# Kernel tuning notes

Measured on AMD Instinct MI355X. Metric: run time of the kernel, lower is better.

## Reference

```python
import jax, jax.numpy as jnp
import numpy as np

HIDDEN = 4096
NUM_BLOCKS = 8
BLOCK = HIDDEN // NUM_BLOCKS  # 512


def setup_inputs() -> dict:
    key = jax.random.key(0)
    k1, k2, k3, k4 = jax.random.split(key, 4)
    return {
        "weight": jax.random.normal(k1, (HIDDEN, HIDDEN), dtype=jnp.float32) * 0.02,
        "bias": jax.random.normal(k2, (HIDDEN,), dtype=jnp.float32) * 0.02,
        "x": jax.random.normal(k3, (4, 2048, HIDDEN), dtype=jnp.float32),
        "proj_R": jax.random.normal(k4, (NUM_BLOCKS, BLOCK, BLOCK), dtype=jnp.float32) * 0.02,
        "layer_idx": 0,
    }


def _cayley_batch(A):
    # Q = (I - S) @ inv(I + S + 1e-6*I), S = 0.5*(A - A^T), batched over blocks
    r = A.shape[-1]
    I = jnp.eye(r, dtype=A.dtype)
    S = 0.5 * (A - jnp.swapaxes(A, -2, -1))
    Minv = jnp.linalg.inv(I + S + 1e-6 * I)
    return jnp.einsum('bij,bjk->bik', I - S, Minv)


def reference(weight, bias, x, proj_R, layer_idx):
    Q = _cayley_batch(proj_R)                     # [nb, bs, bs], orthogonal blocks
    nb, bs, _ = Q.shape
    # block_diag(Q) @ weight == batched block-row matmul (off-diagonal blocks are zero)
    Wb = weight.reshape(nb, bs, weight.shape[1])  # [nb, bs, in]
    filt = jnp.einsum('bij,bjk->bik', Q, Wb).reshape(nb * bs, weight.shape[1])
    # F.linear(x, filt, bias)
    return jnp.einsum('bsi,oi->bso', x, filt) + bias
```

## Files before the change

### kernel.cpp

```cpp
#include <hip/hip_runtime.h>

typedef unsigned short u16;
typedef __attribute__((ext_vector_type(8))) short bf16x8;
typedef __attribute__((ext_vector_type(4))) float f32x4;
typedef __attribute__((ext_vector_type(8))) unsigned short u16x8;
typedef __attribute__((ext_vector_type(4))) unsigned short u16x4;

__device__ __forceinline__ u16 f2bf(float f){
  unsigned int u = __builtin_bit_cast(unsigned int, f);
  u += 0x7FFFu + ((u >> 16) & 1u);
  return (u16)(u >> 16);
}
__device__ __forceinline__ float bf2f(u16 h){
  unsigned int u = ((unsigned int)h) << 16;
  return __builtin_bit_cast(float, u);
}

__device__ __forceinline__ void load16(const u16* g, u16* s){
  __builtin_amdgcn_global_load_lds((const __attribute__((address_space(1))) unsigned int*)g,
                                   (__attribute__((address_space(3))) unsigned int*)s,
                                   16, 0, 0);
}

__global__ __launch_bounds__(256) void build_s(const float* __restrict__ R, u16* __restrict__ Sbf,
                                               u16* __restrict__ Dbf){
  int idx = blockIdx.x * 256 + threadIdx.x;
  int b = idx >> 18;
  int i = (idx >> 9) & 511;
  int j = idx & 511;
  float a  = R[idx];
  float at = R[(b << 18) + (j << 9) + i];
  float s = 0.5f * (a - at);
  Sbf[idx] = f2bf(s);
  Dbf[idx] = f2bf((i == j ? 2.000003f : 0.0f) - 2.000001f * s);
}

__global__ __launch_bounds__(256) void conv_bf16(const float* __restrict__ src, u16* __restrict__ dst){
  size_t i = (size_t)blockIdx.x * 256 + threadIdx.x;
  const float4* s = (const float4*)src + i * 2;
  float4 v0 = s[0], v1 = s[1];
  u16x8 o = { f2bf(v0.x), f2bf(v0.y), f2bf(v0.z), f2bf(v0.w),
              f2bf(v1.x), f2bf(v1.y), f2bf(v1.z), f2bf(v1.w) };
  *(u16x8*)(dst + i * 8) = o;
}

__global__ __launch_bounds__(256) void transpose_w(const float* __restrict__ W, u16* __restrict__ Wt){
  const int b = blockIdx.z;
  const int i0 = blockIdx.x << 5;
  const int j0 = blockIdx.y << 5;
  __shared__ float tile[32][33];
  const int t = threadIdx.x;
  const int r = t >> 3, c = (t & 7) << 2;
  float4 v = *(const float4*)&W[(size_t)((b << 9) + j0 + r) * 4096 + i0 + c];
  tile[r][c+0] = v.x; tile[r][c+1] = v.y; tile[r][c+2] = v.z; tile[r][c+3] = v.w;
  __syncthreads();
  u16x4 o = { f2bf(tile[c+0][r]), f2bf(tile[c+1][r]), f2bf(tile[c+2][r]), f2bf(tile[c+3][r]) };
  *(u16x4*)&Wt[((size_t)b << 21) + (size_t)(i0 + r) * 512 + j0 + c] = o;
}

template<int EPI>
__global__ __launch_bounds__(256) void gemm_ns(const u16* __restrict__ A, const u16* __restrict__ B,
                                               void* __restrict__ Cout, void* __restrict__ aux,
                                               void* __restrict__ aux2,
                                               int M, int N, int K){
  const int bz = blockIdx.z;
  const char* Ab = (const char*)(A + (size_t)bz * M * K);
  const char* Bb = (const char*)(B + (size_t)bz * N * K);
  const int m0 = blockIdx.y << 6, n0 = blockIdx.x << 6;
  __shared__ __align__(16) char As[4096];
  __shared__ __align__(16) char Bs[4096];
  const int t = threadIdx.x;
  const int w = t >> 6, l = t & 63;
  const int wm = w >> 1, wn = w & 1;
  const size_t Kb = (size_t)K << 1;
  const int sR = t >> 2;
  const int sK = ((t ^ (t >> 2)) & 3) << 4;
  const int kq = (((l >> 4) ^ l) & 3) << 4;
  const int aRd = ((wm << 5) + (l & 15)) * 64 + kq;
  const int bRd = ((wn << 5) + (l & 15)) * 64 + kq;
  f32x4 acc[2][2] = {};
  for (int k0 = 0; k0 < K; k0 += 32){
    const size_t kb = (size_t)k0 << 1;
    load16((const u16*)(Ab + (size_t)(m0 + sR) * Kb + kb + sK), (u16*)(As + t * 16));
    load16((const u16*)(Bb + (size_t)(n0 + sR) * Kb + kb + sK), (u16*)(Bs + t * 16));
    __syncthreads();
    bf16x8 aF[2], bF[2];
#pragma unroll
    for (int mf = 0; mf < 2; ++mf) aF[mf] = *(const bf16x8*)(As + aRd + (mf << 10));
#pragma unroll
    for (int nf = 0; nf < 2; ++nf) bF[nf] = *(const bf16x8*)(Bs + bRd + (nf << 10));
#pragma unroll
    for (int mf = 0; mf < 2; ++mf)
#pragma unroll
      for (int nf = 0; nf < 2; ++nf)
        acc[mf][nf] = __builtin_amdgcn_mfma_f32_16x16x32_bf16(aF[mf], bF[nf], acc[mf][nf], 0, 0, 0);
    __syncthreads();
  }
#pragma unroll
  for (int mf = 0; mf < 2; ++mf){
#pragma unroll
    for (int nf = 0; nf < 2; ++nf){
      const int col = n0 + (wn << 5) + (nf << 4) + (l & 15);
#pragma unroll
      for (int q = 0; q < 4; ++q){
        const int row = m0 + (wm << 5) + (mf << 4) + ((l >> 4) << 2) + q;
        float v = acc[mf][nf][q];
        size_t gi = ((size_t)bz * M + row) * N + col;
        size_t g2 = (((size_t)bz * M + row) << 10) + col;
        if (EPI == 2){
          ((u16*)Cout)[gi] = f2bf(v);
        } else if (EPI == 3){
          ((u16*)Cout)[gi] = f2bf((row == col ? 2.0f : 0.0f) - v);
        } else if (EPI == 9){
          ((u16*)Cout)[gi] = f2bf(v - (row == col ? 1.0f : 0.0f));
        } else {
          float p = v + (row == col ? 1.000002f : 0.0f);
          u16 ph = f2bf(p);
          ((u16*)Cout)[g2] = ph;
          ((u16*)Cout)[g2 + 512] = f2bf(p - bf2f(ph));
          const float beta = 0.8264463f;
          u16 x1 = f2bf((row == col ? 2.0f * beta : 0.0f) - beta * beta * p);
          ((u16*)aux)[gi] = x1;
          ((u16*)aux2)[g2] = x1;
          ((u16*)aux2)[g2 + 512] = x1;
        }
      }
    }
  }
}

template<int EPI>
__global__ __launch_bounds__(512, 2) void gemm256(const u16* __restrict__ A, const u16* __restrict__ B,
                                                  void* __restrict__ Cout, const float* __restrict__ aux,
                                                  int M, int N, int K){
  __shared__ __align__(16) char lds[131072];
  const int bz = blockIdx.z;
  const char* Ab = (const char*)(A + (size_t)bz * M * K);
  const char* Bb = (const char*)(B + (size_t)bz * N * K);
  const int NB = N >> 8;
  const int nwg = gridDim.x;
  const int bid = blockIdx.x;
  const int swzb = (bid & 7) * (nwg >> 3) + (bid >> 3);
  const int m0 = (swzb / NB) << 8;
  const int n0 = (swzb % NB) << 8;
  const int tid = threadIdx.x;
  const int w = tid >> 6, l = tid & 63;
  const int wm = w >> 2, wn = w & 3;
  const size_t Kb = (size_t)K << 1;
  const int NT = K >> 6;
  const int sRow = tid >> 3;
  const int sCol = ((tid & 7) << 4) ^ ((sRow & 7) << 4);
  const int sDst = tid << 4;
  const char* aS = Ab + (size_t)(m0 + sRow) * Kb + sCol;
  const char* bS = Bb + (size_t)(n0 + sRow) * Kb + sCol;
  const int lrow = (l & 15) << 7;
  const int kq0 = (((l >> 4) << 4)) ^ ((l & 7) << 4);
  const int aOff = (wm << 14) + lrow;
  const int bOff = 32768 + ((wn >> 1) << 14) + ((wn & 1) << 13) + lrow;

#define STAGE_H(isB, h, tt) { \
    const int _lo = (((tt) & 1) << 16) + ((isB) << 15) + ((h) << 14); \
    const char* _s = ((isB) ? bS : aS) + ((size_t)((h) << 7)) * Kb + ((size_t)(tt) << 7); \
    load16((const u16*)_s, (u16*)(lds + _lo + sDst)); \
    load16((const u16*)(_s + (Kb << 6)), (u16*)(lds + _lo + 8192 + sDst)); }

#define RD_A(bufb, UQ) \
  _Pragma("unroll") for (int i2 = 0; i2 < 4; ++i2){ \
    aF[i2][0] = *(const bf16x8*)(lds + (bufb) + aOff + ((UQ) << 13) + (i2 << 11) + kq0); \
    aF[i2][1] = *(const bf16x8*)(lds + (bufb) + aOff + ((UQ) << 13) + (i2 << 11) + (kq0 ^ 64)); }

#define RD_B(bufb, VQ) \
  _Pragma("unroll") for (int j2 = 0; j2 < 2; ++j2){ \
    bF[VQ][j2][0] = *(const bf16x8*)(lds + (bufb) + bOff + ((VQ) << 12) + (j2 << 11) + kq0); \
    bF[VQ][j2][1] = *(const bf16x8*)(lds + (bufb) + bOff + ((VQ) << 12) + (j2 << 11) + (kq0 ^ 64)); }

#define MFMA16(UQ, VQ) \
    _Pragma("unroll") for (int i2 = 0; i2 < 4; ++i2) \
      _Pragma("unroll") for (int j2 = 0; j2 < 2; ++j2){ \
        acc[(UQ)*4+i2][(VQ)*2+j2] = __builtin_amdgcn_mfma_f32_16x16x32_bf16(aF[i2][0], bF[VQ][j2][0], acc[(UQ)*4+i2][(VQ)*2+j2], 0, 0, 0); \
        acc[(UQ)*4+i2][(VQ)*2+j2] = __builtin_amdgcn_mfma_f32_16x16x32_bf16(aF[i2][1], bF[VQ][j2][1], acc[(UQ)*4+i2][(VQ)*2+j2], 0, 0, 0); }

#define BAR asm volatile("s_barrier" ::: "memory");
#define VM0 asm volatile("s_waitcnt vmcnt(0)" ::: "memory");

  bf16x8 aF[4][2], bF[2][2][2];
  f32x4 acc[8][4] = {};

  STAGE_H(0,0,0) STAGE_H(1,0,0) STAGE_H(0,1,0) STAGE_H(1,1,0)
  VM0 BAR

#define KTILE(t, bufb) { \
    RD_A(bufb, 0) RD_B(bufb, 0) \
    if ((t) + 1 < NT) { STAGE_H(0,0,(t)+1) STAGE_H(1,0,(t)+1) } \
    MFMA16(0,0) \
    RD_B(bufb, 1) \
    if ((t) + 1 < NT) { STAGE_H(0,1,(t)+1) STAGE_H(1,1,(t)+1) } \
    MFMA16(0,1) \
    RD_A(bufb, 1) \
    MFMA16(1,1) \
    MFMA16(1,0) \
    __builtin_amdgcn_sched_barrier(0); \
    VM0 BAR }

#pragma unroll 1
  for (int tp = 0; tp < NT; tp += 2){
    KTILE(tp, 0)
    KTILE(tp+1, 65536)
  }
#undef KTILE
#undef STAGE_H
#undef RD_A
#undef RD_B
#undef MFMA16
#undef BAR
#undef VM0

#pragma unroll
  for (int mf = 0; mf < 8; ++mf){
#pragma unroll
    for (int nf = 0; nf < 4; ++nf){
      const int col = n0 + (wn << 6) + (nf << 4) + (l & 15);
#pragma unroll
      for (int q = 0; q < 4; ++q){
        const int row = m0 + (wm << 7) + (mf << 4) + ((l >> 4) << 2) + q;
        float v = acc[mf][nf][q];
        if (EPI == 0){
          ((float*)Cout)[(size_t)row * N + col] = v + aux[col];
        } else {
          ((u16*)Cout)[((size_t)bz * M + row) * N + col] = f2bf(v);
        }
      }
    }
  }
}

extern "C" void kernel_launch(void* const* d_in, const int* in_sizes, int n_in,
                              void* d_out, int out_size, void* d_ws, size_t ws_size,
                              hipStream_t stream){
  const float* W    = (const float*)d_in[0];
  const float* bias = (const float*)d_in[1];
  const float* x    = (const float*)d_in[2];
  const float* R    = (const float*)d_in[3];
  (void)in_sizes; (void)n_in; (void)out_size; (void)ws_size;

  char* ws = (char*)d_ws;
  const size_t MiB = (size_t)1 << 20;
  u16*   Sbf  = (u16*)(ws + 0 * MiB);
  u16*   Dbf  = (u16*)(ws + 4 * MiB);
  u16*   X1   = (u16*)(ws + 16 * MiB);
  u16*   Ybf  = (u16*)(ws + 20 * MiB);
  u16*   X2   = (u16*)(ws + 24 * MiB);
  u16*   Phl  = (u16*)(ws + 28 * MiB);
  u16*   X1d  = (u16*)(ws + 44 * MiB);
  u16*   G    = Sbf;
  u16*   Wt   = (u16*)(ws + 8 * MiB);
  u16*   filt = (u16*)(ws + 64 * MiB);
  u16*   xbf  = (u16*)(ws + 0 * MiB);

  const dim3 gNS(8, 8, 8);

  build_s<<<8192, 256, 0, stream>>>(R, Sbf, Dbf);
  gemm_ns<11><<<gNS, 256, 0, stream>>>(Sbf, Sbf, Phl, X1, X1d, 512, 512, 512);
  gemm_ns<3><<<gNS, 256, 0, stream>>>(Phl, X1d, Ybf, nullptr, nullptr, 512, 512, 1024);
  gemm_ns<2><<<gNS, 256, 0, stream>>>(X1, Ybf, X2, nullptr, nullptr, 512, 512, 512);
  gemm_ns<9><<<gNS, 256, 0, stream>>>(Dbf, X2, G, nullptr, nullptr, 512, 512, 512);
  transpose_w<<<dim3(128, 16, 8), 256, 0, stream>>>(W, Wt);
  gemm256<2><<<dim3(32, 1, 8), 512, 0, stream>>>(G, Wt, (void*)filt, nullptr, 512, 4096, 512);
  conv_bf16<<<16384, 256, 0, stream>>>(x, xbf);
  gemm256<0><<<dim3(512, 1, 1), 512, 0, stream>>>(xbf, filt, d_out, bias, 8192, 4096, 4096);
}
```

Baseline: 346.6 us.

## Fuse fp32-to-bf16 conversion of x into the main GEMM A-tile staging

Removes the separate conv_bf16 pass over x and adds a new GEMM kernel that loads fp32 activations into registers, converts them to bf16, and writes them into LDS while B still uses direct global-to-LDS loads. This eliminates a full write and re-read of the bf16 copy of x and one kernel launch. In exchange the GEMM reads twice as many bytes for A per tile and uses register-staged loads that need extra waits and registers, which may reduce latency hiding.

```diff
diff --git a/kernel.cpp b/kernel.cpp
--- a/kernel.cpp
+++ b/kernel.cpp
@@ -33,15 +33,6 @@
   float s = 0.5f * (a - at);
   Sbf[idx] = f2bf(s);
   Dbf[idx] = f2bf((i == j ? 2.000003f : 0.0f) - 2.000001f * s);
-}
-
-__global__ __launch_bounds__(256) void conv_bf16(const float* __restrict__ src, u16* __restrict__ dst){
-  size_t i = (size_t)blockIdx.x * 256 + threadIdx.x;
-  const float4* s = (const float4*)src + i * 2;
-  float4 v0 = s[0], v1 = s[1];
-  u16x8 o = { f2bf(v0.x), f2bf(v0.y), f2bf(v0.z), f2bf(v0.w),
-              f2bf(v1.x), f2bf(v1.y), f2bf(v1.z), f2bf(v1.w) };
-  *(u16x8*)(dst + i * 8) = o;
 }
 
 __global__ __launch_bounds__(256) void transpose_w(const float* __restrict__ W, u16* __restrict__ Wt){
@@ -208,12 +199,6 @@
     KTILE(tp+1, 65536)
   }
 #undef KTILE
-#undef STAGE_H
-#undef RD_A
-#undef RD_B
-#undef MFMA16
-#undef BAR
-#undef VM0
 
 #pragma unroll
   for (int mf = 0; mf < 8; ++mf){
@@ -232,6 +217,133 @@
       }
     }
   }
+#undef STAGE_H
+#undef RD_A
+#undef RD_B
+#undef MFMA16
+#undef BAR
+#undef VM0
+}
+
+__global__ __launch_bounds__(512, 2) void gemm256f(const float* __restrict__ Af, const u16* __restrict__ Bw,
+                                                   float* __restrict__ Cout, const float* __restrict__ bias,
+                                                   int M, int N, int K){
+  __shared__ __align__(16) char lds[131072];
+  const char* Bb = (const char*)Bw;
+  const int NB = N >> 8;
+  const int nwg = gridDim.x;
+  const int bid = blockIdx.x;
+  const int swzb = (bid & 7) * (nwg >> 3) + (bid >> 3);
+  const int m0 = (swzb / NB) << 8;
+  const int n0 = (swzb % NB) << 8;
+  const int tid = threadIdx.x;
+  const int w = tid >> 6, l = tid & 63;
+  const int wm = w >> 2, wn = w & 3;
+  const size_t Kb = (size_t)K << 1;
+  const int NT = K >> 6;
+  const int sRow = tid >> 3;
+  const int sCol = ((tid & 7) << 4) ^ ((sRow & 7) << 4);
+  const int sDst = tid << 4;
+  const char* bS = Bb + (size_t)(n0 + sRow) * Kb + sCol;
+  const float* aS = Af + (size_t)(m0 + sRow) * K + (sCol >> 1);
+  const size_t rowK64 = (size_t)64 * K;
+  const int lrow = (l & 15) << 7;
+  const int kq0 = (((l >> 4) << 4)) ^ ((l & 7) << 4);
+  const int aOff = (wm << 14) + lrow;
+  const int bOff = 32768 + ((wn >> 1) << 14) + ((wn & 1) << 13) + lrow;
+
+#define STAGE_B(h, tt) { \
+    const int _lo = (((tt) & 1) << 16) + 32768 + ((h) << 14); \
+    const char* _s = bS + ((size_t)((h) << 7)) * Kb + ((size_t)(tt) << 7); \
+    load16((const u16*)_s, (u16*)(lds + _lo + sDst)); \
+    load16((const u16*)(_s + (Kb << 6)), (u16*)(lds + _lo + 8192 + sDst)); }
+
+#define A_ISSUE(p, tt) { \
+    const float* _a = aS + (size_t)(tt) * 64 + (size_t)((p) << 1) * rowK64; \
+    sa0 = *(const float4*)(_a);           sb0 = *(const float4*)(_a + 4); \
+    sa1 = *(const float4*)(_a + rowK64);  sb1 = *(const float4*)(_a + rowK64 + 4); }
+#define A_WRITE(p, tt) { \
+    const int _lo = (((tt) & 1) << 16) + ((p) << 14); \
+    u16x8 o0 = { f2bf(sa0.x), f2bf(sa0.y), f2bf(sa0.z), f2bf(sa0.w), \
+                 f2bf(sb0.x), f2bf(sb0.y), f2bf(sb0.z), f2bf(sb0.w) }; \
+    *(u16x8*)(lds + _lo + sDst) = o0; \
+    u16x8 o1 = { f2bf(sa1.x), f2bf(sa1.y), f2bf(sa1.z), f2bf(sa1.w), \
+                 f2bf(sb1.x), f2bf(sb1.y), f2bf(sb1.z), f2bf(sb1.w) }; \
+    *(u16x8*)(lds + _lo + 8192 + sDst) = o1; }
+
+#define RD_A(bufb, UQ) \
+  _Pragma("unroll") for (int i2 = 0; i2 < 4; ++i2){ \
+    aF[i2][0] = *(const bf16x8*)(lds + (bufb) + aOff + ((UQ) << 13) + (i2 << 11) + kq0); \
+    aF[i2][1] = *(const bf16x8*)(lds + (bufb) + aOff + ((UQ) << 13) + (i2 << 11) + (kq0 ^ 64)); }
+
+#define RD_B(bufb, VQ) \
+  _Pragma("unroll") for (int j2 = 0; j2 < 2; ++j2){ \
+    bF[VQ][j2][0] = *(const bf16x8*)(lds + (bufb) + bOff + ((VQ) << 12) + (j2 << 11) + kq0); \
+    bF[VQ][j2][1] = *(const bf16x8*)(lds + (bufb) + bOff + ((VQ) << 12) + (j2 << 11) + (kq0 ^ 64)); }
+
+#define MFMA16(UQ, VQ) \
+    _Pragma("unroll") for (int i2 = 0; i2 < 4; ++i2) \
+      _Pragma("unroll") for (int j2 = 0; j2 < 2; ++j2){ \
+        acc[(UQ)*4+i2][(VQ)*2+j2] = __builtin_amdgcn_mfma_f32_16x16x32_bf16(aF[i2][0], bF[VQ][j2][0], acc[(UQ)*4+i2][(VQ)*2+j2], 0, 0, 0); \
+        acc[(UQ)*4+i2][(VQ)*2+j2] = __builtin_amdgcn_mfma_f32_16x16x32_bf16(aF[i2][1], bF[VQ][j2][1], acc[(UQ)*4+i2][(VQ)*2+j2], 0, 0, 0); }
+
+#define BAR asm volatile("s_barrier" ::: "memory");
+#define LGK0 asm volatile("s_waitcnt lgkmcnt(0)" ::: "memory");
+#define VM0 asm volatile("s_waitcnt vmcnt(0)" ::: "memory");
+
+  bf16x8 aF[4][2], bF[2][2][2];
+  float4 sa0, sb0, sa1, sb1;
+  f32x4 acc[8][4] = {};
+
+  A_ISSUE(0, 0) STAGE_B(0, 0) STAGE_B(1, 0)
+  A_WRITE(0, 0)
+  A_ISSUE(1, 0)
+  A_WRITE(1, 0)
+  LGK0 VM0 BAR
+
+#define KTILE(t, bufb) { \
+    if ((t) + 1 < NT) { A_ISSUE(0, (t)+1) STAGE_B(0, (t)+1) } \
+    RD_A(bufb, 0) RD_B(bufb, 0) \
+    MFMA16(0,0) \
+    RD_B(bufb, 1) \
+    if ((t) + 1 < NT) { STAGE_B(1, (t)+1) } \
+    MFMA16(0,1) \
+    if ((t) + 1 < NT) { A_WRITE(0, (t)+1) A_ISSUE(1, (t)+1) } \
+    RD_A(bufb, 1) \
+    MFMA16(1,1) \
+    MFMA16(1,0) \
+    if ((t) + 1 < NT) { A_WRITE(1, (t)+1) } \
+    __builtin_amdgcn_sched_barrier(0); \
+    LGK0 VM0 BAR }
+
+#pragma unroll 1
+  for (int tp = 0; tp < NT; tp += 2){
+    KTILE(tp, 0)
+    KTILE(tp+1, 65536)
+  }
+#undef KTILE
+
+#pragma unroll
+  for (int mf = 0; mf < 8; ++mf){
+#pragma unroll
+    for (int nf = 0; nf < 4; ++nf){
+      const int col = n0 + (wn << 6) + (nf << 4) + (l & 15);
+#pragma unroll
+      for (int q = 0; q < 4; ++q){
+        const int row = m0 + (wm << 7) + (mf << 4) + ((l >> 4) << 2) + q;
+        Cout[(size_t)row * N + col] = acc[mf][nf][q] + bias[col];
+      }
+    }
+  }
+#undef STAGE_B
+#undef A_ISSUE
+#undef A_WRITE
+#undef RD_A
+#undef RD_B
+#undef MFMA16
+#undef BAR
+#undef LGK0
+#undef VM0
 }
 
 extern "C" void kernel_launch(void* const* d_in, const int* in_sizes, int n_in,
@@ -255,7 +367,6 @@
   u16*   G    = Sbf;
   u16*   Wt   = (u16*)(ws + 8 * MiB);
   u16*   filt = (u16*)(ws + 64 * MiB);
-  u16*   xbf  = (u16*)(ws + 0 * MiB);
 
   const dim3 gNS(8, 8, 8);
 
@@ -266,6 +377,5 @@
   gemm_ns<9><<<gNS, 256, 0, stream>>>(Dbf, X2, G, nullptr, nullptr, 512, 512, 512);
   transpose_w<<<dim3(128, 16, 8), 256, 0, stream>>>(W, Wt);
   gemm256<2><<<dim3(32, 1, 8), 512, 0, stream>>>(G, Wt, (void*)filt, nullptr, 512, 4096, 512);
-  conv_bf16<<<16384, 256, 0, stream>>>(x, xbf);
-  gemm256<0><<<dim3(512, 1, 1), 512, 0, stream>>>(xbf, filt, d_out, bias, 8192, 4096, 4096);
-}
+  gemm256f<<<dim3(512, 1, 1), 512, 0, stream>>>(x, filt, (float*)d_out, bias, 8192, 4096, 4096);
+}
```

Result: slower. 422.1 us (+21.8%).
